# Kernel tuning notes

Hardware: AMD Instinct MI355X
Metric: run time of the kernel (lower is better)

Reference implementation:

```python
import jax, jax.numpy as jnp
import numpy as np

N, E, G, H, NF, EF, L = 50000, 800000, 512, 256, 32, 16, 4
BN_EPS = 1e-5


def setup_inputs() -> dict:
    key = jax.random.key(0)
    ks = iter(jax.random.split(key, 40))

    def W(shape, fan_in):
        return (jax.random.normal(next(ks), shape, jnp.float32) / np.sqrt(fan_in)).astype(jnp.float32)

    x = jax.random.normal(next(ks), (N, NF), jnp.float32)
    edge_index = jax.random.randint(next(ks), (2, E), 0, N)
    edge_attr = jax.random.normal(next(ks), (E, EF), jnp.float32)
    batch = jnp.sort(jax.random.randint(next(ks), (N,), 0, G))
    global_feat = jax.random.normal(next(ks), (G, NF), jnp.float32)

    inp = dict(x=x, edge_index=edge_index, edge_attr=edge_attr, batch=batch,
               global_feat=global_feat)
    # input projection
    inp['Win'] = W((NF, H), NF); inp['bin_'] = jnp.zeros((H,), jnp.float32)
    # per-layer GINEConv params (stacked over L layers)
    inp['We'] = W((L, EF, H), EF); inp['be'] = jnp.zeros((L, H), jnp.float32)
    inp['Wl1'] = W((L, H, H), H); inp['bl1'] = jnp.zeros((L, H), jnp.float32)
    inp['Wl2'] = W((L, H, H), H); inp['bl2'] = jnp.zeros((L, H), jnp.float32)
    # BatchNorm (eval mode: running stats)
    inp['bn_w'] = jnp.ones((L, H), jnp.float32); inp['bn_b'] = jnp.zeros((L, H), jnp.float32)
    inp['bn_m'] = jnp.zeros((L, H), jnp.float32); inp['bn_v'] = jnp.ones((L, H), jnp.float32)
    # projection head proj: H -> H//2 -> 64
    inp['Wp1'] = W((H, H // 2), H); inp['bp1'] = jnp.zeros((H // 2,), jnp.float32)
    inp['Wp2'] = W((H // 2, 64), H // 2); inp['bp2'] = jnp.zeros((64,), jnp.float32)
    # fc_final: (H+gfd) -> H -> H//2
    inp['Wf1'] = W((H + NF, H), H + NF); inp['bf1'] = jnp.zeros((H,), jnp.float32)
    inp['Wf2'] = W((H, H // 2), H); inp['bf2'] = jnp.zeros((H // 2,), jnp.float32)
    # edl head: H//2 -> 4
    inp['Whead'] = W((H // 2, 4), H // 2); inp['bhead'] = jnp.zeros((4,), jnp.float32)
    return inp


def reference(x, edge_index, edge_attr, batch, global_feat,
              Win, bin_, We, be, Wl1, bl1, Wl2, bl2,
              bn_w, bn_b, bn_m, bn_v,
              Wp1, bp1, Wp2, bp2, Wf1, bf1, Wf2, bf2, Whead, bhead):
    src, dst = edge_index[0], edge_index[1]
    h = x @ Win + bin_                                  # [N, H]
    for i in range(L):
        e = edge_attr @ We[i] + be[i]                   # [E, H] edge embedding
        msg = jax.nn.relu(h[src] + e)                   # GINEConv message
        aggr = jax.ops.segment_sum(msg, dst, num_segments=N)
        t = h + aggr                                    # (1+eps)*x + aggr, eps=0
        t = jax.nn.relu(t @ Wl1[i] + bl1[i]) @ Wl2[i] + bl2[i]
        t = (t - bn_m[i]) * (bn_w[i] / jnp.sqrt(bn_v[i] + BN_EPS)) + bn_b[i]
        h = h + jax.nn.relu(t)                          # residual
    g = jax.ops.segment_sum(h, batch, num_segments=G)   # global_add_pool [G, H]
    z = jax.nn.relu(g @ Wp1 + bp1) @ Wp2 + bp2          # [G, 64]
    z = z / jnp.maximum(jnp.linalg.norm(z, axis=1, keepdims=True), 1e-12)
    gc = jnp.concatenate([g, global_feat], axis=1)      # [G, H+gfd]
    gf = jax.nn.relu(jax.nn.relu(gc @ Wf1 + bf1) @ Wf2 + bf2)
    o = gf @ Whead + bhead                              # [G, 4]
    gamma = o[:, 0]
    nu = jax.nn.softplus(o[:, 1]) + 1e-6
    alpha = jax.nn.softplus(o[:, 2]) + 1.0 + 1e-6
    beta = jax.nn.softplus(o[:, 3]) + 1e-6
    edl = jnp.stack([gamma, nu, alpha, beta], axis=1)
    return edl, z, g
```

## Files before the change

### kernel.cpp

```cpp
#include <hip/hip_runtime.h>
#include <math.h>

#define N_NODES 50000
#define N_EDGES 800000
#define G_GRAPHS 512
#define H_DIM 256
#define NF_DIM 32
#define EF_DIM 16
#define L_LAYERS 4
#define BN_EPS 1e-5f

typedef __bf16 bf16_t;
typedef __attribute__((ext_vector_type(8))) __bf16 bf16x8;
typedef __attribute__((ext_vector_type(4))) float f32x4;
typedef _Float16 f16_t;
typedef __attribute__((ext_vector_type(2))) _Float16 f16x2;
typedef __attribute__((ext_vector_type(8))) _Float16 f16x8;

union f16x8_pairs {
  f16x8 v;
  f16x2 p[4];
};

__global__ __launch_bounds__(256) void k_init_h(
    const float* __restrict__ x, const float* __restrict__ Win,
    const float* __restrict__ bin, bf16_t* __restrict__ hb) {
  int row = blockIdx.x;
  int c = threadIdx.x;
  __shared__ float xs[NF_DIM];
  if (threadIdx.x < NF_DIM) xs[threadIdx.x] = x[(size_t)row * NF_DIM + threadIdx.x];
  __syncthreads();
  float acc = bin[c];
#pragma unroll
  for (int k = 0; k < NF_DIM; ++k) acc += xs[k] * Win[k * H_DIM + c];
  hb[(size_t)row * H_DIM + c] = (bf16_t)acc;
}

__global__ __launch_bounds__(256) void k_prepW(
    const float* __restrict__ Wl1, const float* __restrict__ Wl2,
    bf16_t* __restrict__ Wt1, bf16_t* __restrict__ Wt2) {
  int n = blockIdx.x;
  int ly = blockIdx.y;
  int k = threadIdx.x;
  const float* W = (ly < L_LAYERS) ? Wl1 : Wl2;
  bf16_t* Wt = (ly < L_LAYERS) ? Wt1 : Wt2;
  int l = ly & 3;
  Wt[(size_t)l * 65536 + n * 256 + k] = (bf16_t)W[(size_t)l * 65536 + k * 256 + n];
}

__global__ __launch_bounds__(256) void k_deg(
    const int* __restrict__ dsts, int* __restrict__ deg) {
  int e = blockIdx.x * 256 + threadIdx.x;
  if (e < N_EDGES) atomicAdd(&deg[dsts[e]], 1);
}

#define SCAN_B 512
__global__ __launch_bounds__(SCAN_B) void k_scan1(
    const int* __restrict__ deg, int* __restrict__ incl, int* __restrict__ bsum) {
  __shared__ int s[SCAN_B];
  int gidx = blockIdx.x * SCAN_B + threadIdx.x;
  int v = (gidx < N_NODES) ? deg[gidx] : 0;
  s[threadIdx.x] = v;
  __syncthreads();
  for (int off = 1; off < SCAN_B; off <<= 1) {
    int t = (threadIdx.x >= off) ? s[threadIdx.x - off] : 0;
    __syncthreads();
    s[threadIdx.x] += t;
    __syncthreads();
  }
  if (gidx < N_NODES) incl[gidx] = s[threadIdx.x];
  if (threadIdx.x == SCAN_B - 1) bsum[blockIdx.x] = s[SCAN_B - 1];
}

__global__ void k_scan2(int* __restrict__ bsum, int nb) {
  if (threadIdx.x == 0 && blockIdx.x == 0) {
    int acc = 0;
    for (int i = 0; i < nb; ++i) { int t = bsum[i]; bsum[i] = acc; acc += t; }
  }
}

__global__ __launch_bounds__(SCAN_B) void k_scan3(
    const int* __restrict__ incl, const int* __restrict__ deg,
    const int* __restrict__ bsum, int* __restrict__ off) {
  int gidx = blockIdx.x * SCAN_B + threadIdx.x;
  if (gidx < N_NODES) off[gidx] = incl[gidx] - deg[gidx] + bsum[blockIdx.x];
  if (gidx == 0) off[N_NODES] = N_EDGES;
}

__global__ __launch_bounds__(256) void k_scatter(
    const int* __restrict__ srcs, const int* __restrict__ dsts,
    const int* __restrict__ off, int* __restrict__ fill,
    int* __restrict__ src_csr, const float* __restrict__ ea,
    f16_t* __restrict__ eac) {
  int e = blockIdx.x * 256 + threadIdx.x;
  if (e < N_EDGES) {
    int d = dsts[e];
    int pos = atomicAdd(&fill[d], 1);
    int idx = off[d] + pos;
    src_csr[idx] = srcs[e];
    const f32x4* p = (const f32x4*)(ea + (size_t)e * EF_DIM);
    f32x4 v0 = p[0], v1 = p[1], v2 = p[2], v3 = p[3];
    f16x8 o0, o1;
    o0[0] = (f16_t)v0.x; o0[1] = (f16_t)v0.y; o0[2] = (f16_t)v0.z; o0[3] = (f16_t)v0.w;
    o0[4] = (f16_t)v1.x; o0[5] = (f16_t)v1.y; o0[6] = (f16_t)v1.z; o0[7] = (f16_t)v1.w;
    o1[0] = (f16_t)v2.x; o1[1] = (f16_t)v2.y; o1[2] = (f16_t)v2.z; o1[3] = (f16_t)v2.w;
    o1[4] = (f16_t)v3.x; o1[5] = (f16_t)v3.y; o1[6] = (f16_t)v3.z; o1[7] = (f16_t)v3.w;
    f16x8* dst = (f16x8*)(eac + (size_t)idx * EF_DIM);
    dst[0] = o0;
    dst[1] = o1;
  }
}

#define AGGR_GRID 12544

__device__ __forceinline__ void edge_dot2(const f16_t* __restrict__ eac,
                                          size_t i, const f16x2* __restrict__ w0,
                                          const f16x2* __restrict__ w1,
                                          float& m0, float& m1) {
  const f16x8* pp = (const f16x8*)(eac + i * EF_DIM);
  f16x8_pairs u0, u1;
  u0.v = pp[0];
  u1.v = pp[1];
#pragma unroll
  for (int j = 0; j < 4; ++j) {
    m0 = __builtin_amdgcn_fdot2(u0.p[j], w0[j], m0, false);
    m1 = __builtin_amdgcn_fdot2(u0.p[j], w1[j], m1, false);
  }
#pragma unroll
  for (int j = 0; j < 4; ++j) {
    m0 = __builtin_amdgcn_fdot2(u1.p[j], w0[j + 4], m0, false);
    m1 = __builtin_amdgcn_fdot2(u1.p[j], w1[j + 4], m1, false);
  }
}

__global__ __launch_bounds__(128) void k_aggr(
    const int* __restrict__ off, const int* __restrict__ src_csr,
    const f16_t* __restrict__ eac, const bf16_t* __restrict__ hb,
    const float* __restrict__ We, const float* __restrict__ be,
    bf16_t* __restrict__ t0b) {
  const int tid = threadIdx.x;
  const int c0 = tid * 2;
  f16x2 w0[8], w1[8];
#pragma unroll
  for (int j = 0; j < 8; ++j) {
    f16x2 t0, t1;
    t0[0] = (f16_t)We[(2 * j) * H_DIM + c0];
    t0[1] = (f16_t)We[(2 * j + 1) * H_DIM + c0];
    t1[0] = (f16_t)We[(2 * j) * H_DIM + c0 + 1];
    t1[1] = (f16_t)We[(2 * j + 1) * H_DIM + c0 + 1];
    w0[j] = t0;
    w1[j] = t1;
  }
  const float be0 = be[c0], be1 = be[c0 + 1];
  const unsigned* __restrict__ hb32 = (const unsigned*)hb;
  for (int n = blockIdx.x; n < N_NODES; n += AGGR_GRID) {
    const int s0 = off[n], s1 = off[n + 1];
    float acc0 = 0.f, acc1 = 0.f;
    int i = s0;
    for (; i + 4 <= s1; i += 4) {
      int sA = src_csr[i], sB = src_csr[i + 1], sC = src_csr[i + 2], sD = src_csr[i + 3];
      unsigned uA = hb32[(unsigned)sA * 128u + tid];
      unsigned uB = hb32[(unsigned)sB * 128u + tid];
      unsigned uC = hb32[(unsigned)sC * 128u + tid];
      unsigned uD = hb32[(unsigned)sD * 128u + tid];
      float mA0 = be0, mA1 = be1, mB0 = be0, mB1 = be1;
      float mC0 = be0, mC1 = be1, mD0 = be0, mD1 = be1;
      edge_dot2(eac, (size_t)i, w0, w1, mA0, mA1);
      edge_dot2(eac, (size_t)i + 1, w0, w1, mB0, mB1);
      edge_dot2(eac, (size_t)i + 2, w0, w1, mC0, mC1);
      edge_dot2(eac, (size_t)i + 3, w0, w1, mD0, mD1);
      acc0 += fmaxf(mA0 + __uint_as_float(uA << 16), 0.f) +
              fmaxf(mB0 + __uint_as_float(uB << 16), 0.f) +
              fmaxf(mC0 + __uint_as_float(uC << 16), 0.f) +
              fmaxf(mD0 + __uint_as_float(uD << 16), 0.f);
      acc1 += fmaxf(mA1 + __uint_as_float(uA & 0xFFFF0000u), 0.f) +
              fmaxf(mB1 + __uint_as_float(uB & 0xFFFF0000u), 0.f) +
              fmaxf(mC1 + __uint_as_float(uC & 0xFFFF0000u), 0.f) +
              fmaxf(mD1 + __uint_as_float(uD & 0xFFFF0000u), 0.f);
    }
    for (; i < s1; ++i) {
      int s = src_csr[i];
      unsigned u = hb32[(unsigned)s * 128u + tid];
      float m0 = be0, m1 = be1;
      edge_dot2(eac, (size_t)i, w0, w1, m0, m1);
      acc0 += fmaxf(m0 + __uint_as_float(u << 16), 0.f);
      acc1 += fmaxf(m1 + __uint_as_float(u & 0xFFFF0000u), 0.f);
    }
    unsigned hu = hb32[(size_t)n * 128 + tid];
    float h0 = __uint_as_float(hu << 16);
    float h1 = __uint_as_float(hu & 0xFFFF0000u);
    union { bf16_t b[2]; unsigned u; } pk;
    pk.b[0] = (bf16_t)(h0 + acc0);
    pk.b[1] = (bf16_t)(h1 + acc1);
    ((unsigned*)t0b)[(size_t)n * 128 + tid] = pk.u;
  }
}

#define FM 64
#define LSTR 40
#define T1STR 264

__global__ __launch_bounds__(512) void k_mlp(
    const bf16_t* __restrict__ t0b, const bf16_t* __restrict__ W1t,
    const bf16_t* __restrict__ W2t, const float* __restrict__ b1,
    const float* __restrict__ b2, const float* __restrict__ bnw,
    const float* __restrict__ bnb, const float* __restrict__ bnm,
    const float* __restrict__ bnv, bf16_t* __restrict__ hb) {
  __shared__ bf16_t As[2][FM * LSTR];
  __shared__ bf16_t T1[FM * T1STR];
  const int tid = threadIdx.x;
  const int bm = blockIdx.x * FM;
  const int lane = tid & 63;
  const int wv = tid >> 6;
  const int wm = (wv & 1) * 32;
  const int wn = (wv >> 1) * 64;
  const int l15 = lane & 15;
  const int kg = lane >> 4;
  const bool stager = tid < 256;
  const int arow = (tid & 255) >> 2, ach = (tid & 3) * 8;
  f32x4 acc[2][4];

#pragma unroll
  for (int m = 0; m < 2; ++m)
#pragma unroll
    for (int n = 0; n < 4; ++n) acc[m][n] = (f32x4){0.f, 0.f, 0.f, 0.f};
  if (stager) {
    int grow = bm + arow;
    f32x4 v = {0.f, 0.f, 0.f, 0.f};
    if (grow < N_NODES) v = *(const f32x4*)&t0b[(size_t)grow * H_DIM + ach];
    *(f32x4*)&As[0][arow * LSTR + ach] = v;
  }
  __syncthreads();
  int p = 0;
  for (int ks = 0; ks < 8; ++ks) {
    const int k0 = ks * 32;
    bf16x8 af[2], bfr[4];
#pragma unroll
    for (int m = 0; m < 2; ++m)
      af[m] = *(const bf16x8*)&As[p][(wm + m * 16 + l15) * LSTR + kg * 8];
    if (ks < 7 && stager) {
      int grow = bm + arow;
      f32x4 v = {0.f, 0.f, 0.f, 0.f};
      if (grow < N_NODES)
        v = *(const f32x4*)&t0b[(size_t)grow * H_DIM + k0 + 32 + ach];
      *(f32x4*)&As[p ^ 1][arow * LSTR + ach] = v;
    }
#pragma unroll
    for (int n = 0; n < 4; ++n)
      bfr[n] = *(const bf16x8*)&W1t[(size_t)(wn + n * 16 + l15) * H_DIM + k0 + kg * 8];
#pragma unroll
    for (int m = 0; m < 2; ++m)
#pragma unroll
      for (int n = 0; n < 4; ++n)
        acc[m][n] =
            __builtin_amdgcn_mfma_f32_16x16x32_bf16(af[m], bfr[n], acc[m][n], 0, 0, 0);
    __syncthreads();
    p ^= 1;
  }
#pragma unroll
  for (int m = 0; m < 2; ++m) {
    int rl0 = wm + m * 16 + kg * 4;
#pragma unroll
    for (int n = 0; n < 4; ++n) {
      int col = wn + n * 16 + l15;
      float bi = b1[col];
#pragma unroll
      for (int r = 0; r < 4; ++r)
        T1[(rl0 + r) * T1STR + col] = (bf16_t)fmaxf(acc[m][n][r] + bi, 0.f);
    }
  }
  __syncthreads();

#pragma unroll
  for (int m = 0; m < 2; ++m)
#pragma unroll
    for (int n = 0; n < 4; ++n) acc[m][n] = (f32x4){0.f, 0.f, 0.f, 0.f};
  for (int ks = 0; ks < 8; ++ks) {
    const int k0 = ks * 32;
    bf16x8 af[2], bfr[4];
#pragma unroll
    for (int m = 0; m < 2; ++m)
      af[m] = *(const bf16x8*)&T1[(wm + m * 16 + l15) * T1STR + k0 + kg * 8];
#pragma unroll
    for (int n = 0; n < 4; ++n)
      bfr[n] = *(const bf16x8*)&W2t[(size_t)(wn + n * 16 + l15) * H_DIM + k0 + kg * 8];
#pragma unroll
    for (int m = 0; m < 2; ++m)
#pragma unroll
      for (int n = 0; n < 4; ++n)
        acc[m][n] =
            __builtin_amdgcn_mfma_f32_16x16x32_bf16(af[m], bfr[n], acc[m][n], 0, 0, 0);
  }
#pragma unroll
  for (int m = 0; m < 2; ++m) {
    int row0 = bm + wm + m * 16 + kg * 4;
#pragma unroll
    for (int n = 0; n < 4; ++n) {
      int col = wn + n * 16 + l15;
      float bi = b2[col];
      float sc = bnw[col] * rsqrtf(bnv[col] + BN_EPS);
      float mu = bnm[col];
      float sb = bnb[col];
#pragma unroll
      for (int r = 0; r < 4; ++r) {
        int rr = row0 + r;
        if (rr < N_NODES) {
          float v = (acc[m][n][r] + bi - mu) * sc + sb;
          size_t o = (size_t)rr * H_DIM + col;
          float old = (float)hb[o];
          hb[o] = (bf16_t)(old + fmaxf(v, 0.f));
        }
      }
    }
  }
}

__global__ __launch_bounds__(512) void k_pool(
    const int* __restrict__ batch, const bf16_t* __restrict__ hb,
    float* __restrict__ g, float* __restrict__ out_g) {
  int gid = blockIdx.x;
  int cp = threadIdx.x & 127;
  int rl = threadIdx.x >> 7;
  int lo = 0, hi = N_NODES;
  while (lo < hi) { int mid = (lo + hi) >> 1; if (batch[mid] < gid) lo = mid + 1; else hi = mid; }
  int start = lo;
  int lo2 = start, hi2 = N_NODES;
  while (lo2 < hi2) { int mid = (lo2 + hi2) >> 1; if (batch[mid] < gid + 1) lo2 = mid + 1; else hi2 = mid; }
  int end = lo2;
  const unsigned* hb32 = (const unsigned*)hb;
  float a0 = 0.f, a1 = 0.f;
  for (int n = start + rl; n < end; n += 4) {
    unsigned u = hb32[(size_t)n * 128 + cp];
    a0 += __uint_as_float(u << 16);
    a1 += __uint_as_float(u & 0xFFFF0000u);
  }
  __shared__ float red[4][H_DIM];
  red[rl][2 * cp] = a0;
  red[rl][2 * cp + 1] = a1;
  __syncthreads();
  if (rl == 0) {
    float s0 = red[0][2 * cp] + red[1][2 * cp] + red[2][2 * cp] + red[3][2 * cp];
    float s1 = red[0][2 * cp + 1] + red[1][2 * cp + 1] + red[2][2 * cp + 1] + red[3][2 * cp + 1];
    g[(size_t)gid * H_DIM + 2 * cp] = s0;
    g[(size_t)gid * H_DIM + 2 * cp + 1] = s1;
    out_g[(size_t)gid * H_DIM + 2 * cp] = s0;
    out_g[(size_t)gid * H_DIM + 2 * cp + 1] = s1;
  }
}

__device__ __forceinline__ float softplusf(float x) {
  return fmaxf(x, 0.f) + log1pf(expf(-fabsf(x)));
}

__global__ __launch_bounds__(256) void k_tail(
    const float* __restrict__ g, const float* __restrict__ gf,
    const float* __restrict__ Wp1, const float* __restrict__ bp1,
    const float* __restrict__ Wp2, const float* __restrict__ bp2,
    const float* __restrict__ Wf1, const float* __restrict__ bf1,
    const float* __restrict__ Wf2, const float* __restrict__ bf2,
    const float* __restrict__ Wh, const float* __restrict__ bh,
    float* __restrict__ out) {
  int gid = blockIdx.x;
  int c = threadIdx.x;
  __shared__ float gc[H_DIM + NF_DIM];
  __shared__ float z1[128];
  __shared__ float q1[H_DIM];
  __shared__ float q2[128];
  gc[c] = g[(size_t)gid * H_DIM + c];
  if (c < NF_DIM) gc[H_DIM + c] = gf[(size_t)gid * NF_DIM + c];
  __syncthreads();
  float aq = bf1[c];
#pragma unroll 8
  for (int k = 0; k < H_DIM + NF_DIM; ++k) aq += gc[k] * Wf1[k * H_DIM + c];
  if (c < 128) {
    float a = bp1[c];
#pragma unroll 8
    for (int k = 0; k < H_DIM; ++k) a += gc[k] * Wp1[k * 128 + c];
    z1[c] = fmaxf(a, 0.f);
  }
  q1[c] = fmaxf(aq, 0.f);
  __syncthreads();
  if (c < 64) {
    float a = bp2[c];
#pragma unroll 8
    for (int k = 0; k < 128; ++k) a += z1[k] * Wp2[k * 64 + c];
    float ss = a * a;
#pragma unroll
    for (int o = 32; o; o >>= 1) ss += __shfl_xor(ss, o);
    float nrm = fmaxf(sqrtf(ss), 1e-12f);
    out[2048 + (size_t)gid * 64 + c] = a / nrm;
  }
  if (c < 128) {
    float a = bf2[c];
#pragma unroll 8
    for (int k = 0; k < H_DIM; ++k) a += q1[k] * Wf2[k * 128 + c];
    q2[c] = fmaxf(a, 0.f);
  }
  __syncthreads();
  if (c < 4) {
    float a = bh[c];
#pragma unroll 8
    for (int k = 0; k < 128; ++k) a += q2[k] * Wh[k * 4 + c];
    float v;
    if (c == 0) v = a;
    else if (c == 2) v = softplusf(a) + 1.f + 1e-6f;
    else v = softplusf(a) + 1e-6f;
    out[(size_t)gid * 4 + c] = v;
  }
}

extern "C" void kernel_launch(void* const* d_in, const int* in_sizes, int n_in,
                              void* d_out, int out_size, void* d_ws, size_t ws_size,
                              hipStream_t stream) {
  const float* x     = (const float*)d_in[0];
  const int*   ei    = (const int*)d_in[1];
  const float* ea    = (const float*)d_in[2];
  const int*   batch = (const int*)d_in[3];
  const float* gf    = (const float*)d_in[4];
  const float* Win   = (const float*)d_in[5];
  const float* bin   = (const float*)d_in[6];
  const float* We    = (const float*)d_in[7];
  const float* be    = (const float*)d_in[8];
  const float* Wl1   = (const float*)d_in[9];
  const float* bl1   = (const float*)d_in[10];
  const float* Wl2   = (const float*)d_in[11];
  const float* bl2   = (const float*)d_in[12];
  const float* bnw   = (const float*)d_in[13];
  const float* bnb   = (const float*)d_in[14];
  const float* bnm   = (const float*)d_in[15];
  const float* bnv   = (const float*)d_in[16];
  const float* Wp1   = (const float*)d_in[17];
  const float* bp1   = (const float*)d_in[18];
  const float* Wp2   = (const float*)d_in[19];
  const float* bp2   = (const float*)d_in[20];
  const float* Wf1   = (const float*)d_in[21];
  const float* bf1   = (const float*)d_in[22];
  const float* Wf2   = (const float*)d_in[23];
  const float* bf2   = (const float*)d_in[24];
  const float* Wh    = (const float*)d_in[25];
  const float* bh    = (const float*)d_in[26];
  float* out = (float*)d_out;

  const int* srcs = ei;
  const int* dsts = ei + N_EDGES;

  const size_t NH = (size_t)N_NODES * H_DIM;
  float* g   = (float*)d_ws;
  f16_t* eac = (f16_t*)(g + (size_t)G_GRAPHS * H_DIM);
  bf16_t* t0b = (bf16_t*)(eac + (size_t)N_EDGES * EF_DIM);
  bf16_t* hb  = t0b + NH;
  bf16_t* Wt1 = hb + NH;
  bf16_t* Wt2 = Wt1 + (size_t)L_LAYERS * 65536;
  int* deg  = (int*)(Wt2 + (size_t)L_LAYERS * 65536);
  int* fill = deg + N_NODES;
  int* incl = fill + N_NODES;
  int* off  = incl + N_NODES;
  int* bsum = off + N_NODES + 1;
  int* src_csr = bsum + 128;

  hipMemsetAsync(deg, 0, N_NODES * sizeof(int), stream);
  hipMemsetAsync(fill, 0, N_NODES * sizeof(int), stream);
  const int nscan = (N_NODES + SCAN_B - 1) / SCAN_B;
  k_deg<<<(N_EDGES + 255) / 256, 256, 0, stream>>>(dsts, deg);
  k_scan1<<<nscan, SCAN_B, 0, stream>>>(deg, incl, bsum);
  k_scan2<<<1, 64, 0, stream>>>(bsum, nscan);
  k_scan3<<<nscan, SCAN_B, 0, stream>>>(incl, deg, bsum, off);
  k_scatter<<<(N_EDGES + 255) / 256, 256, 0, stream>>>(srcs, dsts, off, fill,
                                                       src_csr, ea, eac);
  dim3 wgrid(256, 2 * L_LAYERS);
  k_prepW<<<wgrid, 256, 0, stream>>>(Wl1, Wl2, Wt1, Wt2);
  k_init_h<<<N_NODES, 256, 0, stream>>>(x, Win, bin, hb);

  const int mlpg = (N_NODES + FM - 1) / FM;
  for (int l = 0; l < L_LAYERS; ++l) {
    k_aggr<<<AGGR_GRID, 128, 0, stream>>>(off, src_csr, eac, hb,
                                          We + (size_t)l * EF_DIM * H_DIM,
                                          be + l * H_DIM, t0b);
    k_mlp<<<mlpg, 512, 0, stream>>>(t0b, Wt1 + (size_t)l * 65536,
                                    Wt2 + (size_t)l * 65536, bl1 + l * H_DIM,
                                    bl2 + l * H_DIM, bnw + l * H_DIM,
                                    bnb + l * H_DIM, bnm + l * H_DIM,
                                    bnv + l * H_DIM, hb);
  }

  float* out_g = out + 2048 + (size_t)G_GRAPHS * 64;
  k_pool<<<G_GRAPHS, 512, 0, stream>>>(batch, hb, g, out_g);
  k_tail<<<G_GRAPHS, 256, 0, stream>>>(g, gf, Wp1, bp1, Wp2, bp2, Wf1, bf1,
                                       Wf2, bf2, Wh, bh, out);
}
```

Measured before the change: 899.3 us.

## Fuse edge aggregation and node MLP into one per-layer kernel with ping-pong h

Merges the aggregation kernel and the MLP kernel into a single k_layer kernel. Each 512-thread block aggregates its 64 nodes straight into shared memory, then runs both GEMMs from that buffer, so the t0b intermediate no longer makes a round trip through global memory. Because other blocks still read the previous h, it double-buffers h (hb0/hb1) and swaps them between layers. The cost is that the gather-heavy aggregation now runs under 512-thread blocks with a large shared tile, which can lower occupancy and latency hiding for the irregular gathers. The MLP phase also loses the global-to-LDS double buffering the old version had.

New measurement: 1.260 ms. 40.2% more time.

```diff
diff --git a/kernel.cpp b/kernel.cpp
--- a/kernel.cpp
+++ b/kernel.cpp
@@ -111,7 +111,8 @@
   }
 }
 
-#define AGGR_GRID 12544
+#define FM 64
+#define BSTR 264
 
 __device__ __forceinline__ void edge_dot2(const f16_t* __restrict__ eac,
                                           size_t i, const f16x2* __restrict__ w0,
@@ -133,144 +134,94 @@
   }
 }
 
-__global__ __launch_bounds__(128) void k_aggr(
+__global__ __launch_bounds__(512, 4) void k_layer(
     const int* __restrict__ off, const int* __restrict__ src_csr,
-    const f16_t* __restrict__ eac, const bf16_t* __restrict__ hb,
+    const f16_t* __restrict__ eac, const bf16_t* __restrict__ hbp,
     const float* __restrict__ We, const float* __restrict__ be,
-    bf16_t* __restrict__ t0b) {
-  const int tid = threadIdx.x;
-  const int c0 = tid * 2;
-  f16x2 w0[8], w1[8];
-#pragma unroll
-  for (int j = 0; j < 8; ++j) {
-    f16x2 t0, t1;
-    t0[0] = (f16_t)We[(2 * j) * H_DIM + c0];
-    t0[1] = (f16_t)We[(2 * j + 1) * H_DIM + c0];
-    t1[0] = (f16_t)We[(2 * j) * H_DIM + c0 + 1];
-    t1[1] = (f16_t)We[(2 * j + 1) * H_DIM + c0 + 1];
-    w0[j] = t0;
-    w1[j] = t1;
-  }
-  const float be0 = be[c0], be1 = be[c0 + 1];
-  const unsigned* __restrict__ hb32 = (const unsigned*)hb;
-  for (int n = blockIdx.x; n < N_NODES; n += AGGR_GRID) {
-    const int s0 = off[n], s1 = off[n + 1];
-    float acc0 = 0.f, acc1 = 0.f;
-    int i = s0;
-    for (; i + 4 <= s1; i += 4) {
-      int sA = src_csr[i], sB = src_csr[i + 1], sC = src_csr[i + 2], sD = src_csr[i + 3];
-      unsigned uA = hb32[(unsigned)sA * 128u + tid];
-      unsigned uB = hb32[(unsigned)sB * 128u + tid];
-      unsigned uC = hb32[(unsigned)sC * 128u + tid];
-      unsigned uD = hb32[(unsigned)sD * 128u + tid];
-      float mA0 = be0, mA1 = be1, mB0 = be0, mB1 = be1;
-      float mC0 = be0, mC1 = be1, mD0 = be0, mD1 = be1;
-      edge_dot2(eac, (size_t)i, w0, w1, mA0, mA1);
-      edge_dot2(eac, (size_t)i + 1, w0, w1, mB0, mB1);
-      edge_dot2(eac, (size_t)i + 2, w0, w1, mC0, mC1);
-      edge_dot2(eac, (size_t)i + 3, w0, w1, mD0, mD1);
-      acc0 += fmaxf(mA0 + __uint_as_float(uA << 16), 0.f) +
-              fmaxf(mB0 + __uint_as_float(uB << 16), 0.f) +
-              fmaxf(mC0 + __uint_as_float(uC << 16), 0.f) +
-              fmaxf(mD0 + __uint_as_float(uD << 16), 0.f);
-      acc1 += fmaxf(mA1 + __uint_as_float(uA & 0xFFFF0000u), 0.f) +
-              fmaxf(mB1 + __uint_as_float(uB & 0xFFFF0000u), 0.f) +
-              fmaxf(mC1 + __uint_as_float(uC & 0xFFFF0000u), 0.f) +
-              fmaxf(mD1 + __uint_as_float(uD & 0xFFFF0000u), 0.f);
-    }
-    for (; i < s1; ++i) {
-      int s = src_csr[i];
-      unsigned u = hb32[(unsigned)s * 128u + tid];
-      float m0 = be0, m1 = be1;
-      edge_dot2(eac, (size_t)i, w0, w1, m0, m1);
-      acc0 += fmaxf(m0 + __uint_as_float(u << 16), 0.f);
-      acc1 += fmaxf(m1 + __uint_as_float(u & 0xFFFF0000u), 0.f);
-    }
-    unsigned hu = hb32[(size_t)n * 128 + tid];
-    float h0 = __uint_as_float(hu << 16);
-    float h1 = __uint_as_float(hu & 0xFFFF0000u);
-    union { bf16_t b[2]; unsigned u; } pk;
-    pk.b[0] = (bf16_t)(h0 + acc0);
-    pk.b[1] = (bf16_t)(h1 + acc1);
-    ((unsigned*)t0b)[(size_t)n * 128 + tid] = pk.u;
-  }
-}
-
-#define FM 64
-#define LSTR 40
-#define T1STR 264
-
-__global__ __launch_bounds__(512) void k_mlp(
-    const bf16_t* __restrict__ t0b, const bf16_t* __restrict__ W1t,
-    const bf16_t* __restrict__ W2t, const float* __restrict__ b1,
-    const float* __restrict__ b2, const float* __restrict__ bnw,
-    const float* __restrict__ bnb, const float* __restrict__ bnm,
-    const float* __restrict__ bnv, bf16_t* __restrict__ hb) {
-  __shared__ bf16_t As[2][FM * LSTR];
-  __shared__ bf16_t T1[FM * T1STR];
+    const bf16_t* __restrict__ W1t, const bf16_t* __restrict__ W2t,
+    const float* __restrict__ b1, const float* __restrict__ b2,
+    const float* __restrict__ bnw, const float* __restrict__ bnb,
+    const float* __restrict__ bnm, const float* __restrict__ bnv,
+    bf16_t* __restrict__ hbn) {
+  __shared__ bf16_t buf[FM * BSTR];
   const int tid = threadIdx.x;
   const int bm = blockIdx.x * FM;
+
+  {
+    const int grp = tid >> 7;
+    const int gt = tid & 127;
+    const int c0 = gt * 2;
+    f16x2 w0[8], w1[8];
+#pragma unroll
+    for (int j = 0; j < 8; ++j) {
+      f16x2 t0, t1;
+      t0[0] = (f16_t)We[(2 * j) * H_DIM + c0];
+      t0[1] = (f16_t)We[(2 * j + 1) * H_DIM + c0];
+      t1[0] = (f16_t)We[(2 * j) * H_DIM + c0 + 1];
+      t1[1] = (f16_t)We[(2 * j + 1) * H_DIM + c0 + 1];
+      w0[j] = t0;
+      w1[j] = t1;
+    }
+    const float be0 = be[c0], be1 = be[c0 + 1];
+    const unsigned* __restrict__ hb32 = (const unsigned*)hbp;
+    for (int r = 0; r < 16; ++r) {
+      const int lrow = grp * 16 + r;
+      const int n = bm + lrow;
+      unsigned outv = 0u;
+      if (n < N_NODES) {
+        const int s0 = off[n], s1 = off[n + 1];
+        float acc0 = 0.f, acc1 = 0.f;
+        int i = s0;
+        for (; i + 4 <= s1; i += 4) {
+          int sA = src_csr[i], sB = src_csr[i + 1];
+          int sC = src_csr[i + 2], sD = src_csr[i + 3];
+          unsigned uA = hb32[(unsigned)sA * 128u + gt];
+          unsigned uB = hb32[(unsigned)sB * 128u + gt];
+          unsigned uC = hb32[(unsigned)sC * 128u + gt];
+          unsigned uD = hb32[(unsigned)sD * 128u + gt];
+          float mA0 = be0, mA1 = be1, mB0 = be0, mB1 = be1;
+          float mC0 = be0, mC1 = be1, mD0 = be0, mD1 = be1;
+          edge_dot2(eac, (size_t)i, w0, w1, mA0, mA1);
+          edge_dot2(eac, (size_t)i + 1, w0, w1, mB0, mB1);
+          edge_dot2(eac, (size_t)i + 2, w0, w1, mC0, mC1);
+          edge_dot2(eac, (size_t)i + 3, w0, w1, mD0, mD1);
+          acc0 += fmaxf(mA0 + __uint_as_float(uA << 16), 0.f) +
+                  fmaxf(mB0 + __uint_as_float(uB << 16), 0.f) +
+                  fmaxf(mC0 + __uint_as_float(uC << 16), 0.f) +
+                  fmaxf(mD0 + __uint_as_float(uD << 16), 0.f);
+          acc1 += fmaxf(mA1 + __uint_as_float(uA & 0xFFFF0000u), 0.f) +
+                  fmaxf(mB1 + __uint_as_float(uB & 0xFFFF0000u), 0.f) +
+                  fmaxf(mC1 + __uint_as_float(uC & 0xFFFF0000u), 0.f) +
+                  fmaxf(mD1 + __uint_as_float(uD & 0xFFFF0000u), 0.f);
+        }
+        for (; i < s1; ++i) {
+          int s = src_csr[i];
+          unsigned u = hb32[(unsigned)s * 128u + gt];
+          float m0 = be0, m1 = be1;
+          edge_dot2(eac, (size_t)i, w0, w1, m0, m1);
+          acc0 += fmaxf(m0 + __uint_as_float(u << 16), 0.f);
+          acc1 += fmaxf(m1 + __uint_as_float(u & 0xFFFF0000u), 0.f);
+        }
+        unsigned hu = hb32[(size_t)n * 128 + gt];
+        float h0 = __uint_as_float(hu << 16);
+        float h1 = __uint_as_float(hu & 0xFFFF0000u);
+        union { bf16_t b[2]; unsigned u; } pk;
+        pk.b[0] = (bf16_t)(h0 + acc0);
+        pk.b[1] = (bf16_t)(h1 + acc1);
+        outv = pk.u;
+      }
+      ((unsigned*)(buf + lrow * BSTR))[gt] = outv;
+    }
+  }
+  __syncthreads();
+
   const int lane = tid & 63;
   const int wv = tid >> 6;
   const int wm = (wv & 1) * 32;
   const int wn = (wv >> 1) * 64;
   const int l15 = lane & 15;
   const int kg = lane >> 4;
-  const bool stager = tid < 256;
-  const int arow = (tid & 255) >> 2, ach = (tid & 3) * 8;
   f32x4 acc[2][4];
-
-#pragma unroll
-  for (int m = 0; m < 2; ++m)
-#pragma unroll
-    for (int n = 0; n < 4; ++n) acc[m][n] = (f32x4){0.f, 0.f, 0.f, 0.f};
-  if (stager) {
-    int grow = bm + arow;
-    f32x4 v = {0.f, 0.f, 0.f, 0.f};
-    if (grow < N_NODES) v = *(const f32x4*)&t0b[(size_t)grow * H_DIM + ach];
-    *(f32x4*)&As[0][arow * LSTR + ach] = v;
-  }
-  __syncthreads();
-  int p = 0;
-  for (int ks = 0; ks < 8; ++ks) {
-    const int k0 = ks * 32;
-    bf16x8 af[2], bfr[4];
-#pragma unroll
-    for (int m = 0; m < 2; ++m)
-      af[m] = *(const bf16x8*)&As[p][(wm + m * 16 + l15) * LSTR + kg * 8];
-    if (ks < 7 && stager) {
-      int grow = bm + arow;
-      f32x4 v = {0.f, 0.f, 0.f, 0.f};
-      if (grow < N_NODES)
-        v = *(const f32x4*)&t0b[(size_t)grow * H_DIM + k0 + 32 + ach];
-      *(f32x4*)&As[p ^ 1][arow * LSTR + ach] = v;
-    }
-#pragma unroll
-    for (int n = 0; n < 4; ++n)
-      bfr[n] = *(const bf16x8*)&W1t[(size_t)(wn + n * 16 + l15) * H_DIM + k0 + kg * 8];
-#pragma unroll
-    for (int m = 0; m < 2; ++m)
-#pragma unroll
-      for (int n = 0; n < 4; ++n)
-        acc[m][n] =
-            __builtin_amdgcn_mfma_f32_16x16x32_bf16(af[m], bfr[n], acc[m][n], 0, 0, 0);
-    __syncthreads();
-    p ^= 1;
-  }
-#pragma unroll
-  for (int m = 0; m < 2; ++m) {
-    int rl0 = wm + m * 16 + kg * 4;
-#pragma unroll
-    for (int n = 0; n < 4; ++n) {
-      int col = wn + n * 16 + l15;
-      float bi = b1[col];
-#pragma unroll
-      for (int r = 0; r < 4; ++r)
-        T1[(rl0 + r) * T1STR + col] = (bf16_t)fmaxf(acc[m][n][r] + bi, 0.f);
-    }
-  }
-  __syncthreads();
-
 #pragma unroll
   for (int m = 0; m < 2; ++m)
 #pragma unroll
@@ -280,7 +231,42 @@
     bf16x8 af[2], bfr[4];
 #pragma unroll
     for (int m = 0; m < 2; ++m)
-      af[m] = *(const bf16x8*)&T1[(wm + m * 16 + l15) * T1STR + k0 + kg * 8];
+      af[m] = *(const bf16x8*)&buf[(wm + m * 16 + l15) * BSTR + k0 + kg * 8];
+#pragma unroll
+    for (int n = 0; n < 4; ++n)
+      bfr[n] = *(const bf16x8*)&W1t[(size_t)(wn + n * 16 + l15) * H_DIM + k0 + kg * 8];
+#pragma unroll
+    for (int m = 0; m < 2; ++m)
+#pragma unroll
+      for (int n = 0; n < 4; ++n)
+        acc[m][n] =
+            __builtin_amdgcn_mfma_f32_16x16x32_bf16(af[m], bfr[n], acc[m][n], 0, 0, 0);
+  }
+  __syncthreads();
+#pragma unroll
+  for (int m = 0; m < 2; ++m) {
+    int rl0 = wm + m * 16 + kg * 4;
+#pragma unroll
+    for (int n = 0; n < 4; ++n) {
+      int col = wn + n * 16 + l15;
+      float bi = b1[col];
+#pragma unroll
+      for (int r = 0; r < 4; ++r)
+        buf[(rl0 + r) * BSTR + col] = (bf16_t)fmaxf(acc[m][n][r] + bi, 0.f);
+    }
+  }
+  __syncthreads();
+
+#pragma unroll
+  for (int m = 0; m < 2; ++m)
+#pragma unroll
+    for (int n = 0; n < 4; ++n) acc[m][n] = (f32x4){0.f, 0.f, 0.f, 0.f};
+  for (int ks = 0; ks < 8; ++ks) {
+    const int k0 = ks * 32;
+    bf16x8 af[2], bfr[4];
+#pragma unroll
+    for (int m = 0; m < 2; ++m)
+      af[m] = *(const bf16x8*)&buf[(wm + m * 16 + l15) * BSTR + k0 + kg * 8];
 #pragma unroll
     for (int n = 0; n < 4; ++n)
       bfr[n] = *(const bf16x8*)&W2t[(size_t)(wn + n * 16 + l15) * H_DIM + k0 + kg * 8];
@@ -307,8 +293,8 @@
         if (rr < N_NODES) {
           float v = (acc[m][n][r] + bi - mu) * sc + sb;
           size_t o = (size_t)rr * H_DIM + col;
-          float old = (float)hb[o];
-          hb[o] = (bf16_t)(old + fmaxf(v, 0.f));
+          float old = (float)hbp[o];
+          hbn[o] = (bf16_t)(old + fmaxf(v, 0.f));
         }
       }
     }
@@ -447,9 +433,9 @@
   const size_t NH = (size_t)N_NODES * H_DIM;
   float* g   = (float*)d_ws;
   f16_t* eac = (f16_t*)(g + (size_t)G_GRAPHS * H_DIM);
-  bf16_t* t0b = (bf16_t*)(eac + (size_t)N_EDGES * EF_DIM);
-  bf16_t* hb  = t0b + NH;
-  bf16_t* Wt1 = hb + NH;
+  bf16_t* hb0 = (bf16_t*)(eac + (size_t)N_EDGES * EF_DIM);
+  bf16_t* hb1 = hb0 + NH;
+  bf16_t* Wt1 = hb1 + NH;
   bf16_t* Wt2 = Wt1 + (size_t)L_LAYERS * 65536;
   int* deg  = (int*)(Wt2 + (size_t)L_LAYERS * 65536);
   int* fill = deg + N_NODES;
@@ -469,22 +455,25 @@
                                                        src_csr, ea, eac);
   dim3 wgrid(256, 2 * L_LAYERS);
   k_prepW<<<wgrid, 256, 0, stream>>>(Wl1, Wl2, Wt1, Wt2);
-  k_init_h<<<N_NODES, 256, 0, stream>>>(x, Win, bin, hb);
-
-  const int mlpg = (N_NODES + FM - 1) / FM;
+  k_init_h<<<N_NODES, 256, 0, stream>>>(x, Win, bin, hb0);
+
+  const int lgrid = (N_NODES + FM - 1) / FM;
+  bf16_t* hp = hb0;
+  bf16_t* hn = hb1;
   for (int l = 0; l < L_LAYERS; ++l) {
-    k_aggr<<<AGGR_GRID, 128, 0, stream>>>(off, src_csr, eac, hb,
-                                          We + (size_t)l * EF_DIM * H_DIM,
-                                          be + l * H_DIM, t0b);
-    k_mlp<<<mlpg, 512, 0, stream>>>(t0b, Wt1 + (size_t)l * 65536,
-                                    Wt2 + (size_t)l * 65536, bl1 + l * H_DIM,
-                                    bl2 + l * H_DIM, bnw + l * H_DIM,
-                                    bnb + l * H_DIM, bnm + l * H_DIM,
-                                    bnv + l * H_DIM, hb);
+    k_layer<<<lgrid, 512, 0, stream>>>(off, src_csr, eac, hp,
+                                       We + (size_t)l * EF_DIM * H_DIM,
+                                       be + l * H_DIM,
+                                       Wt1 + (size_t)l * 65536,
+                                       Wt2 + (size_t)l * 65536,
+                                       bl1 + l * H_DIM, bl2 + l * H_DIM,
+                                       bnw + l * H_DIM, bnb + l * H_DIM,
+                                       bnm + l * H_DIM, bnv + l * H_DIM, hn);
+    bf16_t* t = hp; hp = hn; hn = t;
   }
 
   float* out_g = out + 2048 + (size_t)G_GRAPHS * 64;
-  k_pool<<<G_GRAPHS, 512, 0, stream>>>(batch, hb, g, out_g);
+  k_pool<<<G_GRAPHS, 512, 0, stream>>>(batch, hp, g, out_g);
   k_tail<<<G_GRAPHS, 256, 0, stream>>>(g, gf, Wp1, bp1, Wp2, bp2, Wf1, bf1,
                                        Wf2, bf2, Wh, bh, out);
 }
```
